# Performance work log

Hardware: AMD Instinct MI355X
Metric: run time of the kernel (lower is better)

Reference implementation:

```python
import jax, jax.numpy as jnp
import numpy as np
from jax.scipy.special import logsumexp

EPS = 0.05        # entropic regularization (Sinkhorn approximation of exact LP WMD)
N_ITERS = 200     # Sinkhorn iterations


def setup_inputs() -> dict:
    key = jax.random.key(0)
    k1, k2, k3 = jax.random.split(key, 3)
    B, M, N, D = 64, 512, 512, 128
    x = jax.random.normal(k1, (B, M, D), dtype=jnp.float32)
    y = jax.random.normal(k2, (B, N, D), dtype=jnp.float32)
    labels = jax.random.uniform(k3, (B,), dtype=jnp.float32)
    return {"x": x, "y": y, "labels": labels}


def _cost_matrix(x, y):
    # D[b,i,j] = sqrt(mean_d (x[b,i]-y[b,j])^2), computed without the [B,M,N,D] intermediate
    d = x.shape[-1]
    xn = jnp.sum(x * x, axis=-1)                       # [B,M]
    yn = jnp.sum(y * y, axis=-1)                       # [B,N]
    xy = jnp.einsum('bmd,bnd->bmn', x, y)              # [B,M,N]
    sq = (xn[:, :, None] + yn[:, None, :] - 2.0 * xy) / d
    return jnp.sqrt(jnp.maximum(sq, 1e-12))


def _sinkhorn_wmd(D):
    # uniform marginals p=1/M, q=1/N; log-domain Sinkhorn
    B, M, N = D.shape
    logp = -jnp.log(jnp.float32(M))
    logq = -jnp.log(jnp.float32(N))
    f0 = jnp.zeros((B, M), D.dtype)
    g0 = jnp.zeros((B, N), D.dtype)

    def step(carry, _):
        f, g = carry
        f = EPS * (logp - logsumexp((g[:, None, :] - D) / EPS, axis=2))  # [B,M]
        g = EPS * (logq - logsumexp((f[:, :, None] - D) / EPS, axis=1))  # [B,N]
        return (f, g), None

    (f, g), _ = jax.lax.scan(step, (f0, g0), None, length=N_ITERS)
    P = jnp.exp((f[:, :, None] + g[:, None, :] - D) / EPS)  # transport plan [B,M,N]
    return jnp.sum(P * D, axis=(1, 2))                      # WMD per sample [B]


def reference(x, y, labels):
    D = _cost_matrix(x, y)
    wmd = _sinkhorn_wmd(D)          # per-sample Word Mover's Distance
    return jnp.mean((wmd - labels) ** 2)  # MSELoss
```

## Files before the change

kernel.cpp:

```cpp
#include <hip/hip_runtime.h>
#include <hip/hip_fp16.h>

#define B_ 64
#define M_ 512
#define N_ 512
#define D_ 128
constexpr float EPS_ = 0.05f;
constexpr float SHIFT_ = 1.25f;
constexpr int NIT_ = 200;

typedef _Float16 h2 __attribute__((ext_vector_type(2)));
typedef float f2 __attribute__((ext_vector_type(2)));

__device__ __forceinline__ unsigned h2u(h2 x) { return __builtin_bit_cast(unsigned, x); }
__device__ __forceinline__ h2 u2h(unsigned x) { return __builtin_bit_cast(h2, x); }

template <bool HI>
__device__ __forceinline__ h2 cvt_h2(unsigned w) {
    f2 f = __builtin_amdgcn_cvt_pk_f32_fp8((int)w, HI);
    return __builtin_bit_cast(h2, __builtin_amdgcn_cvt_pkrtz(f.x, f.y));
}
template <bool HI>
__device__ __forceinline__ f2 cvt_f2(unsigned w) {
    return __builtin_amdgcn_cvt_pk_f32_fp8((int)w, HI);
}

__device__ __forceinline__ float dot2f(h2 a, h2 b, float c) {
#if __has_builtin(__builtin_amdgcn_fdot2)
    return __builtin_amdgcn_fdot2(a, b, c, false);
#else
    return fmaf((float)a.x, (float)b.x, fmaf((float)a.y, (float)b.y, c));
#endif
}

__device__ __forceinline__ float red16(float x) {
    x += __builtin_bit_cast(float, __builtin_amdgcn_mov_dpp(__builtin_bit_cast(int, x), 0xB1, 0xF, 0xF, true));
    x += __builtin_bit_cast(float, __builtin_amdgcn_mov_dpp(__builtin_bit_cast(int, x), 0x4E, 0xF, 0xF, true));
    x += __builtin_bit_cast(float, __builtin_amdgcn_mov_dpp(__builtin_bit_cast(int, x), 0x124, 0xF, 0xF, true));
    x += __builtin_bit_cast(float, __builtin_amdgcn_mov_dpp(__builtin_bit_cast(int, x), 0x128, 0xF, 0xF, true));
    return x;
}

__global__ __launch_bounds__(256) void wmd_norms(const float* __restrict__ x,
                                                 const float* __restrict__ y,
                                                 float* __restrict__ xn,
                                                 float* __restrict__ yn) {
    int gw = (int)((blockIdx.x * blockDim.x + threadIdx.x) >> 6);
    int l = threadIdx.x & 63;
    const float* src; float* dst; int row;
    if (gw < B_ * M_) { src = x; dst = xn; row = gw; }
    else              { src = y; dst = yn; row = gw - B_ * M_; }
    float2 a = ((const float2*)(src + (size_t)row * D_))[l];
    float s = a.x * a.x + a.y * a.y;
#pragma unroll
    for (int off = 32; off; off >>= 1) s += __shfl_xor(s, off);
    if (l == 0) dst[row] = s;
}

__global__ __launch_bounds__(256) void wmd_build_k(const float* __restrict__ x,
                                                   const float* __restrict__ y,
                                                   const float* __restrict__ xn,
                                                   const float* __restrict__ yn,
                                                   unsigned char* __restrict__ Kp) {
    int b = blockIdx.z, it = blockIdx.y, jt = blockIdx.x;
    __shared__ float xs[32][129];
    __shared__ float ys[32][129];
    const float4* xb = (const float4*)(x + ((size_t)b * M_ + it * 32) * D_);
    const float4* yb = (const float4*)(y + ((size_t)b * N_ + jt * 32) * D_);
    int t = threadIdx.x;
#pragma unroll
    for (int k = 0; k < 4; ++k) {
        int idx = t + k * 256;
        int r = idx >> 5, c = (idx & 31) * 4;
        float4 vx = xb[idx];
        float4 vy = yb[idx];
        xs[r][c] = vx.x; xs[r][c + 1] = vx.y; xs[r][c + 2] = vx.z; xs[r][c + 3] = vx.w;
        ys[r][c] = vy.x; ys[r][c + 1] = vy.y; ys[r][c + 2] = vy.z; ys[r][c + 3] = vy.w;
    }
    __syncthreads();
    int ti = t >> 5, tj = t & 31;
    float a0 = 0.f, a1 = 0.f, a2 = 0.f, a3 = 0.f;
    for (int d = 0; d < D_; ++d) {
        float yv = ys[tj][d];
        a0 += xs[ti][d] * yv;
        a1 += xs[ti + 8][d] * yv;
        a2 += xs[ti + 16][d] * yv;
        a3 += xs[ti + 24][d] * yv;
    }
    float ynj = yn[(size_t)b * N_ + jt * 32 + tj];
    float accs[4] = {a0, a1, a2, a3};
#pragma unroll
    for (int k = 0; k < 4; ++k) {
        int gi = it * 32 + ti + 8 * k;
        float sq = (xn[(size_t)b * M_ + gi] + ynj - 2.0f * accs[k]) * (1.0f / D_);
        float Dv = sqrtf(fmaxf(sq, 1e-12f));
        float kv = fminf(expf((SHIFT_ - Dv) * (1.0f / EPS_)), 448.0f);
        unsigned r8 = (unsigned)__builtin_amdgcn_cvt_pk_fp8_f32(kv, kv, 0, false);
        Kp[((size_t)b * M_ + gi) * N_ + jt * 32 + tj] = (unsigned char)(r8 & 0xff);
    }
}

__global__ __launch_bounds__(1024, 4) void wmd_sinkhorn(const unsigned char* __restrict__ K8,
                                                        float* __restrict__ wmd) {
    int b = blockIdx.x;
    const unsigned char* Kb = K8 + (size_t)b * M_ * N_;
    __shared__ h2 mrg[64][264];
    __shared__ h2 v_sh[256];
    __shared__ float wsum[16];
    int t = threadIdx.x, w = t >> 6, l = t & 63;
    int sub = l & 15, rg = l >> 4;
    const float pmarg = 1.0f / M_;

    uint2 kr[32];
    {
        const unsigned char* base = Kb + ((size_t)(w * 32 + rg) * N_) + sub * 8;
#pragma unroll
        for (int g = 0; g < 8; ++g)
#pragma unroll
            for (int c = 0; c < 4; ++c)
                kr[g * 4 + c] = *(const uint2*)(base + g * 4 * N_ + c * 128);
    }

    h2 vh[16];
    float u_f[8];
    _Float16 one = (_Float16)1.0f;
#pragma unroll
    for (int j = 0; j < 16; ++j) vh[j] = (h2){one, one};

#pragma unroll 1
    for (int it = 0; it < NIT_; ++it) {
        h2 ca[16];
        _Float16 z = (_Float16)0.0f;
#pragma unroll
        for (int j = 0; j < 16; ++j) ca[j] = (h2){z, z};

#pragma unroll
        for (int g = 0; g < 8; ++g) {
            float d0 = 0.f, d1 = 0.f, d2 = 0.f, d3 = 0.f;
#pragma unroll
            for (int c = 0; c < 4; ++c) {
                unsigned lo = kr[g * 4 + c].x, hi = kr[g * 4 + c].y;
                d0 = dot2f(cvt_h2<false>(lo), vh[4 * c + 0], d0);
                d1 = dot2f(cvt_h2<true>(lo),  vh[4 * c + 1], d1);
                d2 = dot2f(cvt_h2<false>(hi), vh[4 * c + 2], d2);
                d3 = dot2f(cvt_h2<true>(hi),  vh[4 * c + 3], d3);
            }
            float dot = red16((d0 + d1) + (d2 + d3));
            float rd = __builtin_amdgcn_rcpf(dot);
            u_f[g] = rd;
            _Float16 uf = (_Float16)rd;
            h2 uh = (h2){uf, uf};
#pragma unroll
            for (int c = 0; c < 4; ++c) {
                unsigned lo = kr[g * 4 + c].x, hi = kr[g * 4 + c].y;
                ca[4 * c + 0] = cvt_h2<false>(lo) * uh + ca[4 * c + 0];
                ca[4 * c + 1] = cvt_h2<true>(lo)  * uh + ca[4 * c + 1];
                ca[4 * c + 2] = cvt_h2<false>(hi) * uh + ca[4 * c + 2];
                ca[4 * c + 3] = cvt_h2<true>(hi)  * uh + ca[4 * c + 3];
            }
        }
        int mr = (w << 2) + rg;
#pragma unroll
        for (int c = 0; c < 4; ++c) {
            uint4 pk = {h2u(ca[4 * c]), h2u(ca[4 * c + 1]), h2u(ca[4 * c + 2]), h2u(ca[4 * c + 3])};
            *(uint4*)&mrg[mr][sub * 4 + 64 * c] = pk;
        }
        __syncthreads();
        {
            int part = rg, cc = sub;
            int col2 = (w << 4) + cc;
            h2 s0 = (h2){z, z}, s1 = (h2){z, z}, s2 = (h2){z, z}, s3 = (h2){z, z};
#pragma unroll
            for (int k = 0; k < 4; ++k) {
                s0 = s0 + mrg[4 * (4 * k + 0) + part][col2];
                s1 = s1 + mrg[4 * (4 * k + 1) + part][col2];
                s2 = s2 + mrg[4 * (4 * k + 2) + part][col2];
                s3 = s3 + mrg[4 * (4 * k + 3) + part][col2];
            }
            h2 s = (s0 + s1) + (s2 + s3);
            s = s + u2h((unsigned)__builtin_amdgcn_ds_swizzle((int)h2u(s), 0x401F));
            s = s + u2h((unsigned)__shfl_xor((int)h2u(s), 32));
            if (l < 16) {
                h2 vv;
                vv.x = (_Float16)__builtin_amdgcn_rcpf((float)s.x);
                vv.y = (_Float16)__builtin_amdgcn_rcpf((float)s.y);
                v_sh[col2] = vv;
            }
        }
        __syncthreads();
#pragma unroll
        for (int c = 0; c < 4; ++c) {
            uint4 vv = *(const uint4*)&v_sh[sub * 4 + 64 * c];
            vh[4 * c + 0] = u2h(vv.x);
            vh[4 * c + 1] = u2h(vv.y);
            vh[4 * c + 2] = u2h(vv.z);
            vh[4 * c + 3] = u2h(vv.w);
        }
    }

    float acc = 0.f;
#pragma unroll
    for (int g = 0; g < 8; ++g) {
        float us = u_f[g];
#pragma unroll
        for (int c = 0; c < 4; ++c) {
            unsigned lo = kr[g * 4 + c].x, hi = kr[g * 4 + c].y;
            f2 kp[4] = {cvt_f2<false>(lo), cvt_f2<true>(lo), cvt_f2<false>(hi), cvt_f2<true>(hi)};
#pragma unroll
            for (int j = 0; j < 4; ++j) {
                h2 vhj = vh[4 * c + j];
                float kx = fmaxf(kp[j].x, 1e-9f), ky = fmaxf(kp[j].y, 1e-9f);
                acc += (us * kx * (float)vhj.x) * (SHIFT_ - EPS_ * __logf(kx));
                acc += (us * ky * (float)vhj.y) * (SHIFT_ - EPS_ * __logf(ky));
            }
        }
    }
#pragma unroll
    for (int off = 1; off < 64; off <<= 1) acc += __shfl_xor(acc, off);
    if (l == 0) wsum[w] = acc;
    __syncthreads();
    if (t == 0) {
        float s = 0.f;
#pragma unroll
        for (int ww = 0; ww < 16; ++ww) s += wsum[ww];
        wmd[b] = s * pmarg;
    }
}

__global__ void wmd_mse(const float* __restrict__ wmd, const float* __restrict__ labels,
                        float* __restrict__ out) {
    int l = threadIdx.x;
    float d = wmd[l] - labels[l];
    d = d * d;
#pragma unroll
    for (int off = 32; off; off >>= 1) d += __shfl_xor(d, off);
    if (l == 0) out[0] = d * (1.0f / B_);
}

extern "C" void kernel_launch(void* const* d_in, const int* in_sizes, int n_in,
                              void* d_out, int out_size, void* d_ws, size_t ws_size,
                              hipStream_t stream) {
    const float* x = (const float*)d_in[0];
    const float* y = (const float*)d_in[1];
    const float* labels = (const float*)d_in[2];
    float* out = (float*)d_out;

    char* ws = (char*)d_ws;
    unsigned char* K8 = (unsigned char*)ws;
    size_t off = (size_t)B_ * M_ * N_;
    float* xn = (float*)(ws + off);        off += (size_t)B_ * M_ * sizeof(float);
    float* yn = (float*)(ws + off);        off += (size_t)B_ * N_ * sizeof(float);
    float* wmd = (float*)(ws + off);

    wmd_norms<<<(B_ * (M_ + N_)) / 4, 256, 0, stream>>>(x, y, xn, yn);
    wmd_build_k<<<dim3(N_ / 32, M_ / 32, B_), 256, 0, stream>>>(x, y, xn, yn, K8);
    wmd_sinkhorn<<<B_, 1024, 0, stream>>>(K8, wmd);
    wmd_mse<<<1, 64, 0, stream>>>(wmd, labels, out);
}
```

Measured before the change: 1.271 ms.

## Halve Sinkhorn block to 512 threads, doubling register-resident K rows per thread

The Sinkhorn kernel now runs 512 threads per batch block instead of 1024, so each thread keeps 16 row-groups of K in registers (uint4 pairs, contiguous 32 bytes per lane) rather than 8. The cross-warp column reduction shrinks to 32 partial rows, is re-indexed so each thread pair sums one column, and needs one xor-shuffle instead of swizzle plus shuffle. Row scalings u move from registers to shared memory for the final cost pass. The aim is fewer waves per block and cheaper barriers and reductions per iteration, in exchange for higher register pressure, more serial work per thread, and only 64 blocks of 512 threads on a large GPU.

```diff
diff --git a/kernel.cpp b/kernel.cpp
--- a/kernel.cpp
+++ b/kernel.cpp
@@ -100,29 +100,29 @@
     }
 }
 
-__global__ __launch_bounds__(1024, 4) void wmd_sinkhorn(const unsigned char* __restrict__ K8,
-                                                        float* __restrict__ wmd) {
+__global__ __launch_bounds__(512, 2) void wmd_sinkhorn(const unsigned char* __restrict__ K8,
+                                                       float* __restrict__ wmd) {
     int b = blockIdx.x;
     const unsigned char* Kb = K8 + (size_t)b * M_ * N_;
-    __shared__ h2 mrg[64][264];
+    __shared__ h2 mrg[32][260];
     __shared__ h2 v_sh[256];
-    __shared__ float wsum[16];
+    __shared__ float u_s[M_];
+    __shared__ float wsum[8];
     int t = threadIdx.x, w = t >> 6, l = t & 63;
     int sub = l & 15, rg = l >> 4;
     const float pmarg = 1.0f / M_;
 
-    uint2 kr[32];
+    uint4 kr[16][2];
     {
-        const unsigned char* base = Kb + ((size_t)(w * 32 + rg) * N_) + sub * 8;
-#pragma unroll
-        for (int g = 0; g < 8; ++g)
-#pragma unroll
-            for (int c = 0; c < 4; ++c)
-                kr[g * 4 + c] = *(const uint2*)(base + g * 4 * N_ + c * 128);
+        const unsigned char* base = Kb + ((size_t)(w * 64 + rg) * N_) + sub * 32;
+#pragma unroll
+        for (int g = 0; g < 16; ++g) {
+            kr[g][0] = *(const uint4*)(base + (size_t)g * 4 * N_);
+            kr[g][1] = *(const uint4*)(base + (size_t)g * 4 * N_ + 16);
+        }
     }
 
     h2 vh[16];
-    float u_f[8];
     _Float16 one = (_Float16)1.0f;
 #pragma unroll
     for (int j = 0; j < 16; ++j) vh[j] = (h2){one, one};
@@ -134,53 +134,55 @@
 #pragma unroll
         for (int j = 0; j < 16; ++j) ca[j] = (h2){z, z};
 
-#pragma unroll
-        for (int g = 0; g < 8; ++g) {
+#pragma unroll 2
+        for (int g = 0; g < 16; ++g) {
+            h2 kh[16];
+#pragma unroll
+            for (int q = 0; q < 2; ++q) {
+                const unsigned* dw = (const unsigned*)&kr[g][q];
+#pragma unroll
+                for (int dd = 0; dd < 4; ++dd) {
+                    kh[q * 8 + dd * 2]     = cvt_h2<false>(dw[dd]);
+                    kh[q * 8 + dd * 2 + 1] = cvt_h2<true>(dw[dd]);
+                }
+            }
             float d0 = 0.f, d1 = 0.f, d2 = 0.f, d3 = 0.f;
 #pragma unroll
-            for (int c = 0; c < 4; ++c) {
-                unsigned lo = kr[g * 4 + c].x, hi = kr[g * 4 + c].y;
-                d0 = dot2f(cvt_h2<false>(lo), vh[4 * c + 0], d0);
-                d1 = dot2f(cvt_h2<true>(lo),  vh[4 * c + 1], d1);
-                d2 = dot2f(cvt_h2<false>(hi), vh[4 * c + 2], d2);
-                d3 = dot2f(cvt_h2<true>(hi),  vh[4 * c + 3], d3);
+            for (int j = 0; j < 4; ++j) {
+                d0 = dot2f(kh[j],      vh[j],      d0);
+                d1 = dot2f(kh[4 + j],  vh[4 + j],  d1);
+                d2 = dot2f(kh[8 + j],  vh[8 + j],  d2);
+                d3 = dot2f(kh[12 + j], vh[12 + j], d3);
             }
             float dot = red16((d0 + d1) + (d2 + d3));
             float rd = __builtin_amdgcn_rcpf(dot);
-            u_f[g] = rd;
+            if (sub == 0) u_s[w * 64 + g * 4 + rg] = rd;
             _Float16 uf = (_Float16)rd;
             h2 uh = (h2){uf, uf};
 #pragma unroll
-            for (int c = 0; c < 4; ++c) {
-                unsigned lo = kr[g * 4 + c].x, hi = kr[g * 4 + c].y;
-                ca[4 * c + 0] = cvt_h2<false>(lo) * uh + ca[4 * c + 0];
-                ca[4 * c + 1] = cvt_h2<true>(lo)  * uh + ca[4 * c + 1];
-                ca[4 * c + 2] = cvt_h2<false>(hi) * uh + ca[4 * c + 2];
-                ca[4 * c + 3] = cvt_h2<true>(hi)  * uh + ca[4 * c + 3];
-            }
+            for (int j = 0; j < 16; ++j) ca[j] = kh[j] * uh + ca[j];
         }
         int mr = (w << 2) + rg;
 #pragma unroll
         for (int c = 0; c < 4; ++c) {
             uint4 pk = {h2u(ca[4 * c]), h2u(ca[4 * c + 1]), h2u(ca[4 * c + 2]), h2u(ca[4 * c + 3])};
-            *(uint4*)&mrg[mr][sub * 4 + 64 * c] = pk;
+            *(uint4*)&mrg[mr][sub * 16 + 4 * c] = pk;
         }
         __syncthreads();
         {
-            int part = rg, cc = sub;
-            int col2 = (w << 4) + cc;
-            h2 s0 = (h2){z, z}, s1 = (h2){z, z}, s2 = (h2){z, z}, s3 = (h2){z, z};
+            int col2 = t >> 1, half = t & 1;
+            _Float16 z2 = (_Float16)0.0f;
+            h2 s0 = (h2){z2, z2}, s1 = (h2){z2, z2}, s2 = (h2){z2, z2}, s3 = (h2){z2, z2};
 #pragma unroll
             for (int k = 0; k < 4; ++k) {
-                s0 = s0 + mrg[4 * (4 * k + 0) + part][col2];
-                s1 = s1 + mrg[4 * (4 * k + 1) + part][col2];
-                s2 = s2 + mrg[4 * (4 * k + 2) + part][col2];
-                s3 = s3 + mrg[4 * (4 * k + 3) + part][col2];
+                s0 = s0 + mrg[half * 16 + k][col2];
+                s1 = s1 + mrg[half * 16 + 4 + k][col2];
+                s2 = s2 + mrg[half * 16 + 8 + k][col2];
+                s3 = s3 + mrg[half * 16 + 12 + k][col2];
             }
             h2 s = (s0 + s1) + (s2 + s3);
-            s = s + u2h((unsigned)__builtin_amdgcn_ds_swizzle((int)h2u(s), 0x401F));
-            s = s + u2h((unsigned)__shfl_xor((int)h2u(s), 32));
-            if (l < 16) {
+            s = s + u2h((unsigned)__shfl_xor((int)h2u(s), 1));
+            if (half == 0) {
                 h2 vv;
                 vv.x = (_Float16)__builtin_amdgcn_rcpf((float)s.x);
                 vv.y = (_Float16)__builtin_amdgcn_rcpf((float)s.y);
@@ -189,29 +191,38 @@
         }
         __syncthreads();
 #pragma unroll
-        for (int c = 0; c < 4; ++c) {
-            uint4 vv = *(const uint4*)&v_sh[sub * 4 + 64 * c];
-            vh[4 * c + 0] = u2h(vv.x);
-            vh[4 * c + 1] = u2h(vv.y);
-            vh[4 * c + 2] = u2h(vv.z);
-            vh[4 * c + 3] = u2h(vv.w);
+        for (int q = 0; q < 2; ++q) {
+            uint4 vv = *(const uint4*)&v_sh[sub * 16 + q * 8];
+            vh[q * 8 + 0] = u2h(vv.x);
+            vh[q * 8 + 1] = u2h(vv.y);
+            vh[q * 8 + 2] = u2h(vv.z);
+            vh[q * 8 + 3] = u2h(vv.w);
+            uint4 vv2 = *(const uint4*)&v_sh[sub * 16 + q * 8 + 4];
+            vh[q * 8 + 4] = u2h(vv2.x);
+            vh[q * 8 + 5] = u2h(vv2.y);
+            vh[q * 8 + 6] = u2h(vv2.z);
+            vh[q * 8 + 7] = u2h(vv2.w);
         }
     }
 
     float acc = 0.f;
-#pragma unroll
-    for (int g = 0; g < 8; ++g) {
-        float us = u_f[g];
-#pragma unroll
-        for (int c = 0; c < 4; ++c) {
-            unsigned lo = kr[g * 4 + c].x, hi = kr[g * 4 + c].y;
-            f2 kp[4] = {cvt_f2<false>(lo), cvt_f2<true>(lo), cvt_f2<false>(hi), cvt_f2<true>(hi)};
-#pragma unroll
-            for (int j = 0; j < 4; ++j) {
-                h2 vhj = vh[4 * c + j];
-                float kx = fmaxf(kp[j].x, 1e-9f), ky = fmaxf(kp[j].y, 1e-9f);
-                acc += (us * kx * (float)vhj.x) * (SHIFT_ - EPS_ * __logf(kx));
-                acc += (us * ky * (float)vhj.y) * (SHIFT_ - EPS_ * __logf(ky));
+#pragma unroll 2
+    for (int g = 0; g < 16; ++g) {
+        float us = u_s[w * 64 + g * 4 + rg];
+#pragma unroll
+        for (int q = 0; q < 2; ++q) {
+            const unsigned* dw = (const unsigned*)&kr[g][q];
+#pragma unroll
+            for (int dd = 0; dd < 4; ++dd) {
+                f2 klo = cvt_f2<false>(dw[dd]);
+                f2 khi = cvt_f2<true>(dw[dd]);
+                h2 v0 = vh[q * 8 + dd * 2], v1 = vh[q * 8 + dd * 2 + 1];
+                float kx = fmaxf(klo.x, 1e-9f), ky = fmaxf(klo.y, 1e-9f);
+                acc += (us * kx * (float)v0.x) * (SHIFT_ - EPS_ * __logf(kx));
+                acc += (us * ky * (float)v0.y) * (SHIFT_ - EPS_ * __logf(ky));
+                kx = fmaxf(khi.x, 1e-9f); ky = fmaxf(khi.y, 1e-9f);
+                acc += (us * kx * (float)v1.x) * (SHIFT_ - EPS_ * __logf(kx));
+                acc += (us * ky * (float)v1.y) * (SHIFT_ - EPS_ * __logf(ky));
             }
         }
     }
@@ -222,7 +233,7 @@
     if (t == 0) {
         float s = 0.f;
 #pragma unroll
-        for (int ww = 0; ww < 16; ++ww) s += wsum[ww];
+        for (int ww = 0; ww < 8; ++ww) s += wsum[ww];
         wmd[b] = s * pmarg;
     }
 }
@@ -254,6 +265,6 @@
 
     wmd_norms<<<(B_ * (M_ + N_)) / 4, 256, 0, stream>>>(x, y, xn, yn);
     wmd_build_k<<<dim3(N_ / 32, M_ / 32, B_), 256, 0, stream>>>(x, y, xn, yn, K8);
-    wmd_sinkhorn<<<B_, 1024, 0, stream>>>(K8, wmd);
+    wmd_sinkhorn<<<B_, 512, 0, stream>>>(K8, wmd);
     wmd_mse<<<1, 64, 0, stream>>>(wmd, labels, out);
 }
```

New measurement: 1.876 ms. +47.6%, slower.
